# Performance work log

Measured on AMD Instinct MI355X. Metric: run time of the kernel, lower is better.

The kernel has to match this reference:

```python
import jax, jax.numpy as jnp
import numpy as np

NUM_HEADS = 12
HEAD_DIM = 64
DIM = NUM_HEADS * HEAD_DIM  # 768
WIN = 14
REL = 2 * WIN - 1  # 27


def setup_inputs() -> dict:
    key = jax.random.key(0)
    ks = jax.random.split(key, 7)
    B, N = 256, WIN * WIN
    return {
        "x": jax.random.normal(ks[0], (B, N, DIM), dtype=jnp.float32),
        "qkv_w": jax.random.normal(ks[1], (3 * DIM, DIM), dtype=jnp.float32) * 0.02,
        "qkv_b": jnp.zeros((3 * DIM,), dtype=jnp.float32),
        "rel_pos_h": jax.random.normal(ks[2], (REL, HEAD_DIM), dtype=jnp.float32) * 0.02,
        "rel_pos_w": jax.random.normal(ks[3], (REL, HEAD_DIM), dtype=jnp.float32) * 0.02,
        "proj_w": jax.random.normal(ks[4], (DIM, DIM), dtype=jnp.float32) * 0.02,
        "proj_b": jnp.zeros((DIM,), dtype=jnp.float32),
        "H": WIN,
        "W": WIN,
    }


def _rel_pos_bias(q, rel_pos_h, rel_pos_w, H, W):
    # q: [B, heads, H*W, d] (already scaled). q_shape == k_shape == (H, W), ratios == 1.
    dist_h = jnp.arange(H)[:, None] - jnp.arange(H)[None, :] + (H - 1)  # [H, H]
    dist_w = jnp.arange(W)[:, None] - jnp.arange(W)[None, :] + (W - 1)  # [W, W]
    Rh = rel_pos_h[dist_h]  # [H, H, d]
    Rw = rel_pos_w[dist_w]  # [W, W, d]
    B, nh = q.shape[0], q.shape[1]
    r_q = q.reshape(B, nh, H, W, q.shape[-1])
    rel_h = jnp.einsum("bnhwd,hkd->bnhwk", r_q, Rh)  # [B, nh, H, W, Hk]
    rel_w = jnp.einsum("bnhwd,wkd->bnhwk", r_q, Rw)  # [B, nh, H, W, Wk]
    return rel_h[..., :, None] + rel_w[..., None, :]  # [B, nh, H, W, Hk, Wk]


def reference(x, qkv_w, qkv_b, rel_pos_h, rel_pos_w, proj_w, proj_b, H, W):
    B, N, C = x.shape
    d = C // NUM_HEADS
    scale = d ** -0.5
    qkv = x @ qkv_w.T + qkv_b  # [B, N, 3C]
    qkv = qkv.reshape(B, N, 3, NUM_HEADS, d).transpose(2, 0, 3, 1, 4)
    q, k, v = qkv[0], qkv[1], qkv[2]  # [B, nh, N, d]
    q = q * scale
    attn = jnp.einsum("bhqd,bhkd->bhqk", q, k)  # [B, nh, N, N]
    bias = _rel_pos_bias(q, rel_pos_h, rel_pos_w, H, W)
    attn = (attn.reshape(B, NUM_HEADS, H, W, H, W) + bias).reshape(B, NUM_HEADS, N, N)
    attn = jax.nn.softmax(attn, axis=-1)
    out = jnp.einsum("bhqk,bhkd->bhqd", attn, v)  # [B, nh, N, d]
    out = out.transpose(0, 2, 1, 3).reshape(B, N, C)
    return out @ proj_w.T + proj_b
```

## Files before the change

### kernel.cpp

```cpp
#include <hip/hip_runtime.h>
#include <stdint.h>


typedef __attribute__((ext_vector_type(8))) short bf16x8;
typedef __attribute__((ext_vector_type(4))) float f32x4;
typedef __attribute__((ext_vector_type(4))) unsigned int u32x4;
typedef unsigned short u16;
typedef unsigned int u32;

__device__ __forceinline__ u16 f2bf(float f) {
  u32 x = __float_as_uint(f);
  x += 0x7fffu + ((x >> 16) & 1u);
  return (u16)(x >> 16);
}

__device__ __forceinline__ u32 pack2bf(float a, float b) {
  return (u32)f2bf(a) | ((u32)f2bf(b) << 16);
}

__device__ __forceinline__ void gload_lds16(const void* g, void* l) {
  __builtin_amdgcn_global_load_lds(
      (__attribute__((address_space(1))) void*)g,
      (__attribute__((address_space(3))) void*)l, 16, 0, 0);
}

__global__ __launch_bounds__(256) void cvt_bf16(const float* __restrict__ src,
                                                u16* __restrict__ dst, int n4) {
  int i = blockIdx.x * 256 + threadIdx.x;
  if (i < n4) {
    float4 f = ((const float4*)src)[i];
    uint2 p;
    p.x = pack2bf(f.x, f.y);
    p.y = pack2bf(f.z, f.w);
    ((uint2*)dst)[i] = p;
  }
}

__device__ __forceinline__ void stage8(const u16* pA, const u16* pB,
                                       char* dstA, int k0) {
#pragma unroll
  for (int i = 0; i < 4; i++)
    gload_lds16(pA + (size_t)i * 49152 + k0, dstA + i * 8192);
#pragma unroll
  for (int i = 0; i < 4; i++)
    gload_lds16(pB + (size_t)i * 49152 + k0, dstA + 32768 + i * 8192);
}

template <int MODE, int NT>
__global__ __launch_bounds__(512, 2) void gemm256(
    const u16* __restrict__ A, const u16* __restrict__ W,
    const float* __restrict__ bias, u16* __restrict__ qb, u16* __restrict__ kb,
    u16* __restrict__ vb, float* __restrict__ outf) {
  __shared__ char lds[131072];

  const int t = threadIdx.x;
  const int lane = t & 63, wv = t >> 6;
  const int quad = lane >> 4, l15 = lane & 15;
  const int wm = wv >> 2, wn = wv & 3;

  const u32 nwg = gridDim.x;
  const u32 wg = blockIdx.x;
  const u32 qd = nwg >> 3, rm = nwg & 7;
  const u32 xcd = wg & 7, loc = wg >> 3;
  const u32 swz = (xcd < rm) ? (xcd * (qd + 1) + loc)
                             : (rm * (qd + 1) + (xcd - rm) * qd + loc);
  const int mtile = swz / NT;
  const int ntile = (int)swz - mtile * NT;
  const int m0 = mtile << 8, n0 = ntile << 8;

  const int srow = t >> 3;
  const int scol = ((t & 7) ^ (srow & 7)) << 3;
  const u16* pA = A + (size_t)(m0 + srow) * 768 + scol;
  const u16* pB = W + (size_t)(n0 + srow) * 768 + scol;
  char* sdst = lds + t * 16;

  const int swz0 = ((quad) ^ (l15 & 7)) << 4;
  const int swz1 = ((4 + quad) ^ (l15 & 7)) << 4;
  const int arow = (wm * 128 + l15) * 128;
  const int brow = 32768 + (wn * 64 + l15) * 128;

  f32x4 acc[8][4];
#pragma unroll
  for (int i = 0; i < 8; i++)
#pragma unroll
    for (int j = 0; j < 4; j++) acc[i][j] = (f32x4){0.f, 0.f, 0.f, 0.f};

  stage8(pA, pB, sdst, 0);
  asm volatile("s_waitcnt vmcnt(0)" ::: "memory");
  __builtin_amdgcn_s_barrier();

  bf16x8 af[4][2], bfr[4][2];
  for (int kt = 0; kt < 12; ++kt) {
    char* bufc = lds + ((kt & 1) << 16);
    char* nsdst = sdst + (((kt & 1) ^ 1) << 16);
    const int k0n = (kt + 1) << 6;

#pragma unroll
    for (int mf = 0; mf < 4; mf++) {
      af[mf][0] = *(const bf16x8*)(bufc + arow + mf * 2048 + swz0);
      af[mf][1] = *(const bf16x8*)(bufc + arow + mf * 2048 + swz1);
    }
#pragma unroll
    for (int nf = 0; nf < 2; nf++) {
      bfr[nf][0] = *(const bf16x8*)(bufc + brow + nf * 2048 + swz0);
      bfr[nf][1] = *(const bf16x8*)(bufc + brow + nf * 2048 + swz1);
    }
    if (kt < 11) stage8(pA, pB, nsdst, k0n);
    __builtin_amdgcn_s_barrier();
    asm volatile("s_waitcnt lgkmcnt(0)" ::: "memory");
    __builtin_amdgcn_s_setprio(1);
#pragma unroll
    for (int k = 0; k < 2; k++)
#pragma unroll
      for (int mf = 0; mf < 4; mf++)
#pragma unroll
        for (int nf = 0; nf < 2; nf++)
          acc[mf][nf] = __builtin_amdgcn_mfma_f32_16x16x32_bf16(
              af[mf][k], bfr[nf][k], acc[mf][nf], 0, 0, 0);
    __builtin_amdgcn_s_setprio(0);
    __builtin_amdgcn_s_barrier();

#pragma unroll
    for (int nf = 2; nf < 4; nf++) {
      bfr[nf][0] = *(const bf16x8*)(bufc + brow + nf * 2048 + swz0);
      bfr[nf][1] = *(const bf16x8*)(bufc + brow + nf * 2048 + swz1);
    }
    __builtin_amdgcn_s_barrier();
    asm volatile("s_waitcnt lgkmcnt(0)" ::: "memory");
    __builtin_amdgcn_s_setprio(1);
#pragma unroll
    for (int k = 0; k < 2; k++)
#pragma unroll
      for (int mf = 0; mf < 4; mf++)
#pragma unroll
        for (int nf = 2; nf < 4; nf++)
          acc[mf][nf] = __builtin_amdgcn_mfma_f32_16x16x32_bf16(
              af[mf][k], bfr[nf][k], acc[mf][nf], 0, 0, 0);
    __builtin_amdgcn_s_setprio(0);
    __builtin_amdgcn_s_barrier();

#pragma unroll
    for (int mf = 0; mf < 4; mf++) {
      af[mf][0] = *(const bf16x8*)(bufc + arow + (mf + 4) * 2048 + swz0);
      af[mf][1] = *(const bf16x8*)(bufc + arow + (mf + 4) * 2048 + swz1);
    }
    __builtin_amdgcn_s_barrier();
    asm volatile("s_waitcnt lgkmcnt(0)" ::: "memory");
    __builtin_amdgcn_s_setprio(1);
#pragma unroll
    for (int k = 0; k < 2; k++)
#pragma unroll
      for (int mf = 0; mf < 4; mf++)
#pragma unroll
        for (int nf = 0; nf < 2; nf++)
          acc[mf + 4][nf] = __builtin_amdgcn_mfma_f32_16x16x32_bf16(
              af[mf][k], bfr[nf][k], acc[mf + 4][nf], 0, 0, 0);
    __builtin_amdgcn_s_setprio(0);
    __builtin_amdgcn_s_barrier();

    __builtin_amdgcn_s_setprio(1);
#pragma unroll
    for (int k = 0; k < 2; k++)
#pragma unroll
      for (int mf = 0; mf < 4; mf++)
#pragma unroll
        for (int nf = 2; nf < 4; nf++)
          acc[mf + 4][nf] = __builtin_amdgcn_mfma_f32_16x16x32_bf16(
              af[mf][k], bfr[nf][k], acc[mf + 4][nf], 0, 0, 0);
    __builtin_amdgcn_s_setprio(0);
    asm volatile("s_waitcnt vmcnt(0)" ::: "memory");
    __builtin_amdgcn_s_barrier();
  }

  if (MODE == 0) {
    const int which = n0 / 768;
    u16* dst = (which == 0) ? qb : ((which == 1) ? kb : vb);
    const float sc = (which == 0) ? 0.125f : 1.0f;
    float bs[4];
    size_t hb[4];
#pragma unroll
    for (int nf = 0; nf < 4; nf++) {
      int n = n0 + wn * 64 + nf * 16 + l15;
      int cc = n - which * 768;
      bs[nf] = bias[n];
      hb[nf] = (size_t)(cc >> 6) * 12544 + (size_t)(cc & 63);
    }
#pragma unroll
    for (int mf = 0; mf < 8; mf++) {
#pragma unroll
      for (int r = 0; r < 4; r++) {
        int m = m0 + wm * 128 + mf * 16 + (quad << 2) + r;
        int bb = m / 196;
        int tok = m - bb * 196;
        size_t rb = (size_t)bb * 150528 + (size_t)tok * 64;
#pragma unroll
        for (int nf = 0; nf < 4; nf++)
          dst[rb + hb[nf]] = f2bf((acc[mf][nf][r] + bs[nf]) * sc);
      }
    }
  } else {
    float bs[4];
#pragma unroll
    for (int nf = 0; nf < 4; nf++)
      bs[nf] = bias[n0 + wn * 64 + nf * 16 + l15];
#pragma unroll
    for (int mf = 0; mf < 8; mf++) {
#pragma unroll
      for (int r = 0; r < 4; r++) {
        int m = m0 + wm * 128 + mf * 16 + (quad << 2) + r;
#pragma unroll
        for (int nf = 0; nf < 4; nf++)
          outf[(size_t)m * 768 + (n0 + wn * 64 + nf * 16 + l15)] =
              acc[mf][nf][r] + bs[nf];
      }
    }
  }
}

__global__ __launch_bounds__(256) void attn_fused(
    const u16* __restrict__ qbuf, const u16* __restrict__ kbuf,
    const u16* __restrict__ vbuf, const float* __restrict__ rel_h,
    const float* __restrict__ rel_w, u16* __restrict__ aout) {
  __shared__ u16 Vt[26 * 512];
  __shared__ float TLh[4][17][33];
  __shared__ float TLw[4][28][33];

  const int t = threadIdx.x;
  const int bh = blockIdx.x;
  const int b = bh / 12, h = bh - b * 12;
  const int lane = t & 63, wv = t >> 6;
  const int quad = lane >> 4, l15 = lane & 15;
  const size_t base = (size_t)bh * (196 * 64);

  for (int c = t; c < 196 * 8; c += 256) {
    int row = c >> 3, seg = c & 7;
    uint4 vv = *(const uint4*)(vbuf + base + row * 64 + seg * 8);
    const u16* pv8 = (const u16*)&vv;
    u16* dst = Vt + (row >> 3) * 512 + (row & 7);
#pragma unroll
    for (int e = 0; e < 8; e++) {
      int ee = (e + seg) & 7;
      dst[(seg * 8 + ee) * 8] = pv8[ee];
    }
  }
  for (int i = t; i < 12 * 64; i += 256) {
    int k = 196 + (i >> 6), d = i & 63;
    Vt[(k >> 3) * 512 + d * 8 + (k & 7)] = 0;
  }

  bf16x8 brl[2][2][2];
#pragma unroll
  for (int half = 0; half < 2; half++) {
    const float* relp = half ? rel_w : rel_h;
#pragma unroll
    for (int nt = 0; nt < 2; nt++) {
      int ridx = nt * 16 + l15;
      if (ridx > 26) ridx = 26;
#pragma unroll
      for (int ks = 0; ks < 2; ks++) {
        const float* p = relp + ridx * 64 + ks * 32 + quad * 8;
        float4 f0 = *(const float4*)p;
        float4 f1 = *(const float4*)(p + 4);
        bf16x8 r;
        r[0] = (short)f2bf(f0.x); r[1] = (short)f2bf(f0.y);
        r[2] = (short)f2bf(f0.z); r[3] = (short)f2bf(f0.w);
        r[4] = (short)f2bf(f1.x); r[5] = (short)f2bf(f1.y);
        r[6] = (short)f2bf(f1.z); r[7] = (short)f2bf(f1.w);
        brl[half][nt][ks] = r;
      }
    }
  }
  __syncthreads();

  const u16* kB = kbuf + base;
  const u16* qB = qbuf + base;

  for (int p = wv; p < 7; p += 4) {
    const int qt0 = 2 * p;
    const int h0 = (32 * p) / 14;

    bf16x8 aq0[2], aq1[2];
    int hqv[2], wqv[2], hbv[2];
#pragma unroll
    for (int j = 0; j < 2; j++) {
      int qrl = (qt0 + j) * 16 + l15;
      if (qrl > 195) qrl = 195;
      aq0[j] = *(const bf16x8*)(qB + qrl * 64 + quad * 8);
      aq1[j] = *(const bf16x8*)(qB + qrl * 64 + 32 + quad * 8);
      hqv[j] = qrl / 14;
      wqv[j] = qrl - hqv[j] * 14;
      hbv[j] = hqv[j] + 13 - h0;
    }

#pragma unroll
    for (int j = 0; j < 2; j++) {
#pragma unroll
      for (int half = 0; half < 2; half++) {
#pragma unroll
        for (int nt = 0; nt < 2; nt++) {
          f32x4 tc = (f32x4){0.f, 0.f, 0.f, 0.f};
          tc = __builtin_amdgcn_mfma_f32_16x16x32_bf16(brl[half][nt][0], aq0[j], tc, 0, 0, 0);
          tc = __builtin_amdgcn_mfma_f32_16x16x32_bf16(brl[half][nt][1], aq1[j], tc, 0, 0, 0);
#pragma unroll
          for (int r = 0; r < 4; r++) {
            int r27 = nt * 16 + quad * 4 + r;
            if (half == 0) {
              u32 ihh = (u32)(r27 - h0);
              if (ihh < 17u) TLh[wv][ihh][l15 + 16 * j] = tc[r];
            } else {
              if (r27 < 27) TLw[wv][r27][l15 + 16 * j] = tc[r];
            }
          }
        }
      }
    }

    f32x4 oacc[2][4];
#pragma unroll
    for (int j = 0; j < 2; j++)
#pragma unroll
      for (int dt = 0; dt < 4; dt++) oacc[j][dt] = (f32x4){0.f, 0.f, 0.f, 0.f};
    float sm[2] = {0.f, 0.f};
    const int srcA = l15 + ((quad & 1) << 5);
    const bool hi = (quad >> 1) != 0;

    for (int st = 0; st < 6; st++) {
      u32 pw[2][2][2];
#pragma unroll
      for (int u = 0; u < 2; u++) {
        const int kt = st * 2 + u;
        const int keyl = kt * 16 + l15;
        bf16x8 bk0 = *(const bf16x8*)(kB + keyl * 64 + quad * 8);
        bf16x8 bk1 = *(const bf16x8*)(kB + keyl * 64 + 32 + quad * 8);
        const int key0 = kt * 16 + quad * 4;
        const int hk0 = key0 / 14, wk0 = key0 - 14 * hk0;
#pragma unroll
        for (int j = 0; j < 2; j++) {
          f32x4 s = (f32x4){0.f, 0.f, 0.f, 0.f};
          s = __builtin_amdgcn_mfma_f32_16x16x32_bf16(bk0, aq0[j], s, 0, 0, 0);
          s = __builtin_amdgcn_mfma_f32_16x16x32_bf16(bk1, aq1[j], s, 0, 0, 0);
          float pr[4];
#pragma unroll
          for (int r = 0; r < 4; r++) {
            int cr = (wk0 + r >= 14) ? 1 : 0;
            int hk = hk0 + cr, wk = wk0 + r - 14 * cr;
            float v = s[r] + TLh[wv][hbv[j] - hk][l15 + 16 * j] +
                      TLw[wv][wqv[j] - wk + 13][l15 + 16 * j];
            float pe = __expf(v);
            pr[r] = pe;
            sm[j] += pe;
          }
          pw[j][u][0] = pack2bf(pr[0], pr[1]);
          pw[j][u][1] = pack2bf(pr[2], pr[3]);
        }
      }
      bf16x8 pb[2];
#pragma unroll
      for (int j = 0; j < 2; j++) {
        u32 a0 = __shfl(pw[j][0][0], srcA),      b0 = __shfl(pw[j][1][0], srcA);
        u32 a1 = __shfl(pw[j][0][1], srcA),      b1 = __shfl(pw[j][1][1], srcA);
        u32 a2 = __shfl(pw[j][0][0], srcA + 16), b2 = __shfl(pw[j][1][0], srcA + 16);
        u32 a3 = __shfl(pw[j][0][1], srcA + 16), b3 = __shfl(pw[j][1][1], srcA + 16);
        u32x4 pbw = (u32x4){hi ? b0 : a0, hi ? b1 : a1, hi ? b2 : a2, hi ? b3 : a3};
        pb[j] = __builtin_bit_cast(bf16x8, pbw);
      }
#pragma unroll
      for (int dt = 0; dt < 4; dt++) {
        bf16x8 av = *(const bf16x8*)(Vt + (st * 4 + quad) * 512 + (dt * 16 + l15) * 8);
#pragma unroll
        for (int j = 0; j < 2; j++)
          oacc[j][dt] = __builtin_amdgcn_mfma_f32_16x16x32_bf16(av, pb[j], oacc[j][dt], 0, 0, 0);
      }
    }

    {
      const int keyl = 192 + l15;
      const int keyc = (keyl > 195) ? 195 : keyl;
      bf16x8 bk0 = *(const bf16x8*)(kB + keyc * 64 + quad * 8);
      bf16x8 bk1 = *(const bf16x8*)(kB + keyc * 64 + 32 + quad * 8);
      const int key0 = 192 + quad * 4;
      const int hk0 = key0 / 14, wk0 = key0 - 14 * hk0;
      const bool valid = (quad == 0);
      u32 pwt[2][2];
#pragma unroll
      for (int j = 0; j < 2; j++) {
        f32x4 s = (f32x4){0.f, 0.f, 0.f, 0.f};
        s = __builtin_amdgcn_mfma_f32_16x16x32_bf16(bk0, aq0[j], s, 0, 0, 0);
        s = __builtin_amdgcn_mfma_f32_16x16x32_bf16(bk1, aq1[j], s, 0, 0, 0);
        float pr[4];
#pragma unroll
        for (int r = 0; r < 4; r++) {
          int cr = (wk0 + r >= 14) ? 1 : 0;
          int hk = hk0 + cr, wk = wk0 + r - 14 * cr;
          int ih = hbv[j] - hk; ih = ih < 0 ? 0 : ih;
          int iw = wqv[j] - wk + 13; iw = iw < 0 ? 0 : iw;
          float v = s[r] + TLh[wv][ih][l15 + 16 * j] + TLw[wv][iw][l15 + 16 * j];
          float pe = valid ? __expf(v) : 0.f;
          pr[r] = pe;
          sm[j] += pe;
        }
        pwt[j][0] = pack2bf(pr[0], pr[1]);
        pwt[j][1] = pack2bf(pr[2], pr[3]);
      }
      bf16x8 pb[2];
#pragma unroll
      for (int j = 0; j < 2; j++) {
        u32 a0 = __shfl(pwt[j][0], srcA);
        u32 a1 = __shfl(pwt[j][1], srcA);
        u32 a2 = __shfl(pwt[j][0], srcA + 16);
        u32 a3 = __shfl(pwt[j][1], srcA + 16);
        u32x4 pbw = (u32x4){hi ? 0u : a0, hi ? 0u : a1, hi ? 0u : a2, hi ? 0u : a3};
        pb[j] = __builtin_bit_cast(bf16x8, pbw);
      }
#pragma unroll
      for (int dt = 0; dt < 4; dt++) {
        bf16x8 av = (bf16x8){0, 0, 0, 0, 0, 0, 0, 0};
        if (quad < 2)
          av = *(const bf16x8*)(Vt + (24 + quad) * 512 + (dt * 16 + l15) * 8);
#pragma unroll
        for (int j = 0; j < 2; j++)
          oacc[j][dt] = __builtin_amdgcn_mfma_f32_16x16x32_bf16(av, pb[j], oacc[j][dt], 0, 0, 0);
      }
    }

#pragma unroll
    for (int j = 0; j < 2; j++) {
      float smj = sm[j];
      smj += __shfl_xor(smj, 16, 64);
      smj += __shfl_xor(smj, 32, 64);
      const float inv = 1.0f / smj;
      const int qrow = (qt0 + j) * 16 + l15;
      if (qrow < 196) {
        u16* op = aout + ((size_t)(b * 196 + qrow) * 12 + h) * 64;
#pragma unroll
        for (int dt = 0; dt < 4; dt++) {
          uint2 stv;
          stv.x = pack2bf(oacc[j][dt][0] * inv, oacc[j][dt][1] * inv);
          stv.y = pack2bf(oacc[j][dt][2] * inv, oacc[j][dt][3] * inv);
          *(uint2*)(op + dt * 16 + quad * 4) = stv;
        }
      }
    }
  }
}

extern "C" void kernel_launch(void* const* d_in, const int* in_sizes, int n_in,
                              void* d_out, int out_size, void* d_ws, size_t ws_size,
                              hipStream_t stream) {
  (void)in_sizes; (void)n_in; (void)out_size; (void)ws_size;
  const float* x      = (const float*)d_in[0];
  const float* qkv_w  = (const float*)d_in[1];
  const float* qkv_b  = (const float*)d_in[2];
  const float* rel_h  = (const float*)d_in[3];
  const float* rel_w  = (const float*)d_in[4];
  const float* proj_w = (const float*)d_in[5];
  const float* proj_b = (const float*)d_in[6];
  float* out = (float*)d_out;

  char* ws = (char*)d_ws;
  u16* xbf  = (u16*)(ws);
  u16* qbuf = (u16*)(ws + 77070336);
  u16* kbuf = (u16*)(ws + 154140672);
  u16* vbuf = (u16*)(ws + 231211008);
  u16* wqb  = (u16*)(ws + 308281344);
  u16* wpb  = (u16*)(ws + 311820288);

  cvt_bf16<<<37632, 256, 0, stream>>>(x, xbf, 38535168 / 4);
  cvt_bf16<<<1728, 256, 0, stream>>>(qkv_w, wqb, 1769472 / 4);
  cvt_bf16<<<576, 256, 0, stream>>>(proj_w, wpb, 589824 / 4);

  gemm256<0, 9><<<1764, 512, 0, stream>>>(xbf, wqb, qkv_b, qbuf, kbuf, vbuf,
                                          nullptr);
  attn_fused<<<3072, 256, 0, stream>>>(qbuf, kbuf, vbuf, rel_h, rel_w, xbf);
  gemm256<1, 3><<<588, 512, 0, stream>>>(xbf, wpb, proj_b, nullptr, nullptr,
                                         nullptr, out);
}
```

Before: 798.8 us.

## Fold relative-position bias into QK MFMA via one-hot augmented K operand

Measured after the change: 867.9 us. +8.7%, slower.

```diff
diff --git a/kernel.cpp b/kernel.cpp
--- a/kernel.cpp
+++ b/kernel.cpp
@@ -16,6 +16,12 @@
 
 __device__ __forceinline__ u32 pack2bf(float a, float b) {
   return (u32)f2bf(a) | ((u32)f2bf(b) << 16);
+}
+
+__device__ __forceinline__ u32 cvtpk(float a, float b) {
+  u32 r;
+  asm("v_cvt_pk_bf16_f32 %0, %1, %2" : "=v"(r) : "v"(a), "v"(b));
+  return r;
 }
 
 __device__ __forceinline__ void gload_lds16(const void* g, void* l) {
@@ -222,8 +228,7 @@
     const u16* __restrict__ vbuf, const float* __restrict__ rel_h,
     const float* __restrict__ rel_w, u16* __restrict__ aout) {
   __shared__ u16 Vt[26 * 512];
-  __shared__ float TLh[4][17][33];
-  __shared__ float TLw[4][28][33];
+  __shared__ float TL[4][2][27][16];
 
   const int t = threadIdx.x;
   const int bh = blockIdx.x;
@@ -247,29 +252,6 @@
     int k = 196 + (i >> 6), d = i & 63;
     Vt[(k >> 3) * 512 + d * 8 + (k & 7)] = 0;
   }
-
-  bf16x8 brl[2][2][2];
-#pragma unroll
-  for (int half = 0; half < 2; half++) {
-    const float* relp = half ? rel_w : rel_h;
-#pragma unroll
-    for (int nt = 0; nt < 2; nt++) {
-      int ridx = nt * 16 + l15;
-      if (ridx > 26) ridx = 26;
-#pragma unroll
-      for (int ks = 0; ks < 2; ks++) {
-        const float* p = relp + ridx * 64 + ks * 32 + quad * 8;
-        float4 f0 = *(const float4*)p;
-        float4 f1 = *(const float4*)(p + 4);
-        bf16x8 r;
-        r[0] = (short)f2bf(f0.x); r[1] = (short)f2bf(f0.y);
-        r[2] = (short)f2bf(f0.z); r[3] = (short)f2bf(f0.w);
-        r[4] = (short)f2bf(f1.x); r[5] = (short)f2bf(f1.y);
-        r[6] = (short)f2bf(f1.z); r[7] = (short)f2bf(f1.w);
-        brl[half][nt][ks] = r;
-      }
-    }
-  }
   __syncthreads();
 
   const u16* kB = kbuf + base;
@@ -277,10 +259,9 @@
 
   for (int p = wv; p < 7; p += 4) {
     const int qt0 = 2 * p;
-    const int h0 = (32 * p) / 14;
-
-    bf16x8 aq0[2], aq1[2];
-    int hqv[2], wqv[2], hbv[2];
+
+    bf16x8 aq0[2], aq1[2], aq2[2];
+    int hqv[2], wqv[2];
 #pragma unroll
     for (int j = 0; j < 2; j++) {
       int qrl = (qt0 + j) * 16 + l15;
@@ -289,7 +270,26 @@
       aq1[j] = *(const bf16x8*)(qB + qrl * 64 + 32 + quad * 8);
       hqv[j] = qrl / 14;
       wqv[j] = qrl - hqv[j] * 14;
-      hbv[j] = hqv[j] + 13 - h0;
+    }
+
+    bf16x8 brl[2][2][2];
+#pragma unroll
+    for (int half = 0; half < 2; half++) {
+      const float* relp = half ? rel_w : rel_h;
+#pragma unroll
+      for (int nt = 0; nt < 2; nt++) {
+        int ridx = nt * 16 + l15;
+        if (ridx > 26) ridx = 26;
+#pragma unroll
+        for (int ks = 0; ks < 2; ks++) {
+          const float* pf = relp + ridx * 64 + ks * 32 + quad * 8;
+          float4 f0 = *(const float4*)pf;
+          float4 f1 = *(const float4*)(pf + 4);
+          u32x4 rr = (u32x4){cvtpk(f0.x, f0.y), cvtpk(f0.z, f0.w),
+                             cvtpk(f1.x, f1.y), cvtpk(f1.z, f1.w)};
+          brl[half][nt][ks] = __builtin_bit_cast(bf16x8, rr);
+        }
+      }
     }
 
 #pragma unroll
@@ -304,15 +304,22 @@
 #pragma unroll
           for (int r = 0; r < 4; r++) {
             int r27 = nt * 16 + quad * 4 + r;
-            if (half == 0) {
-              u32 ihh = (u32)(r27 - h0);
-              if (ihh < 17u) TLh[wv][ihh][l15 + 16 * j] = tc[r];
-            } else {
-              if (r27 < 27) TLw[wv][r27][l15 + 16 * j] = tc[r];
-            }
+            if (r27 < 27) TL[wv][half][r27][l15] = tc[r];
           }
         }
       }
+      const int hf = quad >> 1;
+      const int cc = (quad < 2) ? hqv[j] : wqv[j];
+      u32 w4[4];
+#pragma unroll
+      for (int wd = 0; wd < 4; wd++) {
+        int bb0 = (quad & 1) * 8 + wd * 2;
+        int bb1 = bb0 + 1;
+        float v0 = (bb0 < 14) ? TL[wv][hf][cc - bb0 + 13][l15] : 0.f;
+        float v1 = (bb1 < 14) ? TL[wv][hf][cc - bb1 + 13][l15] : 0.f;
+        w4[wd] = cvtpk(v0, v1);
+      }
+      aq2[j] = __builtin_bit_cast(bf16x8, (u32x4){w4[0], w4[1], w4[2], w4[3]});
     }
 
     f32x4 oacc[2][4];
@@ -323,6 +330,7 @@
     float sm[2] = {0.f, 0.f};
     const int srcA = l15 + ((quad & 1) << 5);
     const bool hi = (quad >> 1) != 0;
+    const int d0q = quad * 8;
 
     for (int st = 0; st < 6; st++) {
       u32 pw[2][2][2];
@@ -332,26 +340,28 @@
         const int keyl = kt * 16 + l15;
         bf16x8 bk0 = *(const bf16x8*)(kB + keyl * 64 + quad * 8);
         bf16x8 bk1 = *(const bf16x8*)(kB + keyl * 64 + 32 + quad * 8);
-        const int key0 = kt * 16 + quad * 4;
-        const int hk0 = key0 / 14, wk0 = key0 - 14 * hk0;
+        const int hk = keyl / 14;
+        const int wk16 = 16 + (keyl - 14 * hk);
+        u32 b2[4];
+#pragma unroll
+        for (int wd = 0; wd < 4; wd++) {
+          int d = d0q + wd * 2;
+          u32 lo = (d == hk || d == wk16) ? 0x3F80u : 0u;
+          u32 hh = (d + 1 == hk || d + 1 == wk16) ? 0x3F80u : 0u;
+          b2[wd] = lo | (hh << 16);
+        }
+        bf16x8 bk2 = __builtin_bit_cast(bf16x8, (u32x4){b2[0], b2[1], b2[2], b2[3]});
 #pragma unroll
         for (int j = 0; j < 2; j++) {
           f32x4 s = (f32x4){0.f, 0.f, 0.f, 0.f};
           s = __builtin_amdgcn_mfma_f32_16x16x32_bf16(bk0, aq0[j], s, 0, 0, 0);
           s = __builtin_amdgcn_mfma_f32_16x16x32_bf16(bk1, aq1[j], s, 0, 0, 0);
-          float pr[4];
-#pragma unroll
-          for (int r = 0; r < 4; r++) {
-            int cr = (wk0 + r >= 14) ? 1 : 0;
-            int hk = hk0 + cr, wk = wk0 + r - 14 * cr;
-            float v = s[r] + TLh[wv][hbv[j] - hk][l15 + 16 * j] +
-                      TLw[wv][wqv[j] - wk + 13][l15 + 16 * j];
-            float pe = __expf(v);
-            pr[r] = pe;
-            sm[j] += pe;
-          }
-          pw[j][u][0] = pack2bf(pr[0], pr[1]);
-          pw[j][u][1] = pack2bf(pr[2], pr[3]);
+          s = __builtin_amdgcn_mfma_f32_16x16x32_bf16(bk2, aq2[j], s, 0, 0, 0);
+          float p0 = __expf(s[0]), p1 = __expf(s[1]);
+          float p2 = __expf(s[2]), p3 = __expf(s[3]);
+          sm[j] += (p0 + p1) + (p2 + p3);
+          pw[j][u][0] = cvtpk(p0, p1);
+          pw[j][u][1] = cvtpk(p2, p3);
         }
       }
       bf16x8 pb[2];
@@ -378,8 +388,17 @@
       const int keyc = (keyl > 195) ? 195 : keyl;
       bf16x8 bk0 = *(const bf16x8*)(kB + keyc * 64 + quad * 8);
       bf16x8 bk1 = *(const bf16x8*)(kB + keyc * 64 + 32 + quad * 8);
-      const int key0 = 192 + quad * 4;
-      const int hk0 = key0 / 14, wk0 = key0 - 14 * hk0;
+      const int hk = keyc / 14;
+      const int wk16 = 16 + (keyc - 14 * hk);
+      u32 b2[4];
+#pragma unroll
+      for (int wd = 0; wd < 4; wd++) {
+        int d = d0q + wd * 2;
+        u32 lo = (d == hk || d == wk16) ? 0x3F80u : 0u;
+        u32 hh = (d + 1 == hk || d + 1 == wk16) ? 0x3F80u : 0u;
+        b2[wd] = lo | (hh << 16);
+      }
+      bf16x8 bk2 = __builtin_bit_cast(bf16x8, (u32x4){b2[0], b2[1], b2[2], b2[3]});
       const bool valid = (quad == 0);
       u32 pwt[2][2];
 #pragma unroll
@@ -387,20 +406,16 @@
         f32x4 s = (f32x4){0.f, 0.f, 0.f, 0.f};
         s = __builtin_amdgcn_mfma_f32_16x16x32_bf16(bk0, aq0[j], s, 0, 0, 0);
         s = __builtin_amdgcn_mfma_f32_16x16x32_bf16(bk1, aq1[j], s, 0, 0, 0);
+        s = __builtin_amdgcn_mfma_f32_16x16x32_bf16(bk2, aq2[j], s, 0, 0, 0);
         float pr[4];
 #pragma unroll
         for (int r = 0; r < 4; r++) {
-          int cr = (wk0 + r >= 14) ? 1 : 0;
-          int hk = hk0 + cr, wk = wk0 + r - 14 * cr;
-          int ih = hbv[j] - hk; ih = ih < 0 ? 0 : ih;
-          int iw = wqv[j] - wk + 13; iw = iw < 0 ? 0 : iw;
-          float v = s[r] + TLh[wv][ih][l15 + 16 * j] + TLw[wv][iw][l15 + 16 * j];
-          float pe = valid ? __expf(v) : 0.f;
+          float pe = valid ? __expf(s[r]) : 0.f;
           pr[r] = pe;
           sm[j] += pe;
         }
-        pwt[j][0] = pack2bf(pr[0], pr[1]);
-        pwt[j][1] = pack2bf(pr[2], pr[3]);
+        pwt[j][0] = cvtpk(pr[0], pr[1]);
+        pwt[j][1] = cvtpk(pr[2], pr[3]);
       }
       bf16x8 pb[2];
 #pragma unroll
```
